# Kernel optimization log

Measured on AMD Instinct MI355X. Metric: run time of the kernel, lower is better.

Reference implementation:

```python
import jax, jax.numpy as jnp
import numpy as np
import math

N_EMBD = 1024
N_HEAD = 16
B, T = 2, 2048
MASK_VAL = -10.0  # non-standard soft mask value from original module


def setup_inputs() -> dict:
    key = jax.random.key(0)
    k1, k2, k3 = jax.random.split(key, 3)
    scale = 1.0 / math.sqrt(N_EMBD)
    x = jax.random.normal(k1, (B, T, N_EMBD), dtype=jnp.float32)
    # torch Linear weights: (out_features, in_features)
    w_attn = jax.random.normal(k2, (3 * N_EMBD, N_EMBD), dtype=jnp.float32) * scale
    w_proj = jax.random.normal(k3, (N_EMBD, N_EMBD), dtype=jnp.float32) * scale
    return {"x": x, "w_attn": w_attn, "w_proj": w_proj}


def reference(x, w_attn, w_proj):
    Bsz, Tlen, C = x.shape
    hs = C // N_HEAD
    qkv = jnp.einsum('btc,fc->btf', x, w_attn)  # [B,T,3C]
    q, k, v = jnp.split(qkv, 3, axis=-1)
    # [B,H,T,hs]
    q = q.reshape(Bsz, Tlen, N_HEAD, hs).transpose(0, 2, 1, 3)
    k = k.reshape(Bsz, Tlen, N_HEAD, hs).transpose(0, 2, 1, 3)
    v = v.reshape(Bsz, Tlen, N_HEAD, hs).transpose(0, 2, 1, 3)
    att = jnp.einsum('bhqd,bhkd->bhqk', q, k) * (1.0 / math.sqrt(hs))
    causal = jnp.tril(jnp.ones((Tlen, Tlen), dtype=bool))
    att = jnp.where(causal[None, None], att, MASK_VAL)
    att = jax.nn.softmax(att, axis=-1)
    y = jnp.einsum('bhqk,bhkd->bhqd', att, v)
    y = y.transpose(0, 2, 1, 3).reshape(Bsz, Tlen, C)
    return jnp.einsum('btc,fc->btf', y, w_proj)
```

## Files before the change

kernel.cpp:

```cpp
#include <hip/hip_runtime.h>
#include <hip/hip_bf16.h>
#include <stdint.h>

#define BSZ   2
#define TT    2048
#define NH    16
#define HS    64
#define CC    1024
#define C3    3072
#define MT    4096
#define E10   4.5399929762484854e-05f
#define SCL2  0.1803368801111204f

typedef __bf16 bf16;
typedef __bf16 bf16x8 __attribute__((ext_vector_type(8)));
typedef float  f32x4  __attribute__((ext_vector_type(4)));
typedef short  s16x4  __attribute__((ext_vector_type(4)));

#define AS1 __attribute__((address_space(1)))
#define AS3 __attribute__((address_space(3)))

__device__ __forceinline__ void glds16(const bf16* g, bf16* l) {
    __builtin_amdgcn_global_load_lds((const AS1 void*)g, (AS3 void*)l, 16, 0, 0);
}

#define NX8  (MT * CC / 8)
#define NWA8 (C3 * CC / 8)
#define NWP8 (CC * CC / 8)
__global__ __launch_bounds__(256)
void convert_all(const float* __restrict__ x, const float* __restrict__ wa,
                 const float* __restrict__ wp, bf16* __restrict__ xd,
                 bf16* __restrict__ wad, bf16* __restrict__ wpd,
                 int* __restrict__ flag) {
    __shared__ int wsum[4];
    const int tid = threadIdx.x;
    const uint16_t* x16 = (const uint16_t*)x;
    int local = 0;
    {
        uint16_t u = x16[tid];
        int e = (u >> 7) & 0xFF; local += (e >= 96 && e <= 159);
        u = x16[tid + 256];
        e = (u >> 7) & 0xFF; local += (e >= 96 && e <= 159);
    }
    local += __shfl_xor(local, 1, 64);
    local += __shfl_xor(local, 2, 64);
    local += __shfl_xor(local, 4, 64);
    local += __shfl_xor(local, 8, 64);
    local += __shfl_xor(local, 16, 64);
    local += __shfl_xor(local, 32, 64);
    if ((tid & 63) == 0) wsum[tid >> 6] = local;
    __syncthreads();
    const int cnt = wsum[0] + wsum[1] + wsum[2] + wsum[3];
    const int f = (cnt >= 461) ? 0 : 1;
    if (blockIdx.x == 0 && tid == 0) *flag = f;
    if (f == 0) return;

    long i = (long)blockIdx.x * 256 + tid;
    const float* s; bf16* d; long off;
    if (i < NX8)             { s = x;  d = xd;  off = i; }
    else if (i < NX8 + NWA8) { s = wa; d = wad; off = i - NX8; }
    else                     { s = wp; d = wpd; off = i - NX8 - NWA8; }
    const float4* sp = reinterpret_cast<const float4*>(s) + off * 2;
    float4 a = sp[0], b = sp[1];
    bf16x8 r;
    r[0] = (bf16)a.x; r[1] = (bf16)a.y; r[2] = (bf16)a.z; r[3] = (bf16)a.w;
    r[4] = (bf16)b.x; r[5] = (bf16)b.y; r[6] = (bf16)b.z; r[7] = (bf16)b.w;
    reinterpret_cast<bf16x8*>(d)[off] = r;
}

__global__ __launch_bounds__(256)
void gemm_bt(const bf16* __restrict__ A0, const bf16* __restrict__ A1,
             const bf16* __restrict__ B0, const bf16* __restrict__ B1,
             void* __restrict__ Cmain, bf16* __restrict__ Cv,
             float* __restrict__ Vtile,
             const int* __restrict__ flag,
             int M, int N, int K, int lda, int ldb, int ldc,
             int split_col, int cf32_dyn) {
    __shared__ bf16 As[2][128 * 32];
    __shared__ bf16 Bs[2][128 * 32];

    const int f = *flag;
    const bf16* A = f ? A1 : A0;
    const bf16* B = f ? B1 : B0;
    const int cf32 = cf32_dyn & f;

    const int tid  = threadIdx.x;
    const int lane = tid & 63;
    const int wave = tid >> 6;
    const int wm   = wave >> 1;
    const int wn   = wave & 1;
    const int quad = lane >> 4;
    const int l16  = lane & 15;

    const int row0 = blockIdx.y * 128;
    const int col0 = blockIdx.x * 128;

    const int srow = tid >> 2;
    const int skk  = (tid & 3) * 8;

    const bf16* Ap = A + (long)(row0 + srow) * lda + skk;
    const bf16* Bp = B + (long)(col0 + srow) * ldb + skk;

    auto stage = [&](int k0, int buf) {
        glds16(Ap + k0,                  &As[buf][wave * 512]);
        glds16(Ap + (long)64 * lda + k0, &As[buf][wave * 512 + 2048]);
        glds16(Bp + k0,                  &Bs[buf][wave * 512]);
        glds16(Bp + (long)64 * ldb + k0, &Bs[buf][wave * 512 + 2048]);
    };

    f32x4 acc[4][4] = {};
    stage(0, 0);

    for (int k0 = 0; k0 < K; k0 += 32) {
        const int buf = (k0 >> 5) & 1;
        __syncthreads();
        if (k0 + 32 < K) stage(k0 + 32, buf ^ 1);

        const bf16* Ac = As[buf];
        const bf16* Bc = Bs[buf];
        bf16x8 af[4], bfv[4];
#pragma unroll
        for (int mi = 0; mi < 4; ++mi)
            af[mi] = *reinterpret_cast<const bf16x8*>(&Ac[(wm * 64 + mi * 16 + l16) * 32 + quad * 8]);
#pragma unroll
        for (int ni = 0; ni < 4; ++ni)
            bfv[ni] = *reinterpret_cast<const bf16x8*>(&Bc[(wn * 64 + ni * 16 + l16) * 32 + quad * 8]);
#pragma unroll
        for (int mi = 0; mi < 4; ++mi)
#pragma unroll
            for (int ni = 0; ni < 4; ++ni)
                acc[mi][ni] = __builtin_amdgcn_mfma_f32_16x16x32_bf16(af[mi], bfv[ni], acc[mi][ni], 0, 0, 0);
    }

    if (split_col < 0 || col0 < split_col) {
#pragma unroll
        for (int mi = 0; mi < 4; ++mi)
#pragma unroll
            for (int ni = 0; ni < 4; ++ni)
#pragma unroll
                for (int r = 0; r < 4; ++r) {
                    int row = row0 + wm * 64 + mi * 16 + quad * 4 + r;
                    int col = col0 + wn * 64 + ni * 16 + l16;
                    float v = acc[mi][ni][r];
                    if (cf32) ((float*)Cmain)[(long)row * ldc + col] = v;
                    else      ((bf16*)Cmain)[(long)row * ldc + col] = (bf16)v;
                }
    } else {
        const int h  = (col0 - split_col + wn * 64) >> 6;
        const int bq = row0 >> 11;
        const int tc = ((row0 & 2047) >> 6) + wm;
#pragma unroll
        for (int ni = 0; ni < 4; ++ni) {
            long vrow = (long)(bq * NH + h) * 64 + ni * 16 + l16;
#pragma unroll
            for (int mi = 0; mi < 4; ++mi) {
                bf16 outv[4];
#pragma unroll
                for (int r = 0; r < 4; ++r) outv[r] = (bf16)acc[mi][ni][r];
                *reinterpret_cast<uint2*>(&Cv[vrow * 2048 + tc * 64 + quad * 16 + mi * 4]) =
                    *reinterpret_cast<uint2*>(outv);
            }
        }
#pragma unroll
        for (int ni = 0; ni < 4; ++ni) {
            float s = 0.f;
#pragma unroll
            for (int mi = 0; mi < 4; ++mi)
#pragma unroll
                for (int r = 0; r < 4; ++r) s += acc[mi][ni][r];
            s += __shfl_xor(s, 16, 64);
            s += __shfl_xor(s, 32, 64);
            if (quad == 0)
                Vtile[((long)(bq * NH + h) * 32 + tc) * 64 + ni * 16 + l16] = s;
        }
    }
}

__global__ __launch_bounds__(256)
void gemm_bt64(const bf16* __restrict__ A0, const bf16* __restrict__ A1,
               const bf16* __restrict__ B0, const bf16* __restrict__ B1,
               void* __restrict__ C, const int* __restrict__ flag,
               int M, int N, int K, int lda, int ldb, int ldc, int cf32_dyn) {
    __shared__ bf16 As[2][128 * 32];
    __shared__ bf16 Bs[2][64 * 32];

    const int f = *flag;
    const bf16* A = f ? A1 : A0;
    const bf16* B = f ? B1 : B0;
    const int cf32 = cf32_dyn & f;

    const int tid  = threadIdx.x;
    const int lane = tid & 63;
    const int wave = tid >> 6;
    const int wm   = wave >> 1;
    const int wn   = wave & 1;
    const int quad = lane >> 4;
    const int l16  = lane & 15;

    const int row0 = blockIdx.y * 128;
    const int col0 = blockIdx.x * 64;

    const int srow = tid >> 2;
    const int skk  = (tid & 3) * 8;

    const bf16* Ap = A + (long)(row0 + srow) * lda + skk;
    const bf16* Bp = B + (long)(col0 + srow) * ldb + skk;

    auto stage = [&](int k0, int buf) {
        glds16(Ap + k0,                  &As[buf][wave * 512]);
        glds16(Ap + (long)64 * lda + k0, &As[buf][wave * 512 + 2048]);
        glds16(Bp + k0,                  &Bs[buf][wave * 512]);
    };

    f32x4 acc[4][2] = {};
    stage(0, 0);

    for (int k0 = 0; k0 < K; k0 += 32) {
        const int buf = (k0 >> 5) & 1;
        __syncthreads();
        if (k0 + 32 < K) stage(k0 + 32, buf ^ 1);

        const bf16* Ac = As[buf];
        const bf16* Bc = Bs[buf];
        bf16x8 af[4], bfv[2];
#pragma unroll
        for (int mi = 0; mi < 4; ++mi)
            af[mi] = *reinterpret_cast<const bf16x8*>(&Ac[(wm * 64 + mi * 16 + l16) * 32 + quad * 8]);
#pragma unroll
        for (int ni = 0; ni < 2; ++ni)
            bfv[ni] = *reinterpret_cast<const bf16x8*>(&Bc[(wn * 32 + ni * 16 + l16) * 32 + quad * 8]);
#pragma unroll
        for (int mi = 0; mi < 4; ++mi)
#pragma unroll
            for (int ni = 0; ni < 2; ++ni)
                acc[mi][ni] = __builtin_amdgcn_mfma_f32_16x16x32_bf16(af[mi], bfv[ni], acc[mi][ni], 0, 0, 0);
    }

#pragma unroll
    for (int mi = 0; mi < 4; ++mi)
#pragma unroll
        for (int ni = 0; ni < 2; ++ni)
#pragma unroll
            for (int r = 0; r < 4; ++r) {
                int row = row0 + wm * 64 + mi * 16 + quad * 4 + r;
                int col = col0 + wn * 32 + ni * 16 + l16;
                float v = acc[mi][ni][r];
                if (cf32) ((float*)C)[(long)row * ldc + col] = v;
                else      ((bf16*)C)[(long)row * ldc + col] = (bf16)v;
            }
}

__global__ void vts_suffix(const float* __restrict__ Vtile, float* __restrict__ Vts) {
    const int bh = blockIdx.x, d = threadIdx.x;
    Vts[((long)bh * 33 + 32) * 64 + d] = 0.f;
    float acc = 0.f;
    for (int kt = 31; kt >= 0; --kt) {
        acc += Vtile[((long)bh * 32 + kt) * 64 + d];
        Vts[((long)bh * 33 + kt) * 64 + d] = acc;
    }
}

__global__ __launch_bounds__(256, 3)
void attn(bf16* __restrict__ qk, const bf16* __restrict__ Vt,
          const float* __restrict__ Vts) {
    __shared__ bf16 Ks[3][64 * 64];
    __shared__ bf16 Vs[3][64 * 64];

    const int tid  = threadIdx.x;
    const int lane = tid & 63;
    const int wave = tid >> 6;
    const int quad = lane >> 4;
    const int l16  = lane & 15;

    const int f2   = blockIdx.x;
    const int xcd  = f2 & 7;
    const int slot = f2 >> 3;
    const int u    = slot & 3;
    const int chunk = 31 - (slot >> 2);
    const int h = xcd * 2 + (u & 1);
    const int b = u >> 1;
    const int bh = b * 16 + h;
    const int q0 = chunk * 64;
    const long rbase = (long)b * TT;
    const int ktend = chunk + 1;

    const bf16* qp = qk + (rbase + q0 + wave * 16 + l16) * 2048 + h * HS;
    bf16x8 qf0 = *reinterpret_cast<const bf16x8*>(qp + quad * 8);
    bf16x8 qf1 = *reinterpret_cast<const bf16x8*>(qp + 32 + quad * 8);

    f32x4 O[4] = {};
    float lp = 0.f;

    const int rl  = lane >> 3;
    const int cs  = (lane & 7) ^ rl;
    const int row0dma = wave * 16 + rl;
    const bf16* kgb = qk + (rbase + row0dma) * 2048 + CC + h * HS + cs * 8;
    const bf16* vgb = Vt + ((long)(b * NH + h) * 64 + row0dma) * 2048 + cs * 8;
    const int sx = l16 & 7;

    auto stage = [&](int kt, int bi) {
        glds16(kgb + (long)(kt * 64) * 2048,     &Ks[bi][wave * 1024]);
        glds16(kgb + (long)(kt * 64 + 8) * 2048, &Ks[bi][wave * 1024 + 512]);
        glds16(vgb + kt * 64,                    &Vs[bi][wave * 1024]);
        glds16(vgb + 8 * 2048 + kt * 64,         &Vs[bi][wave * 1024 + 512]);
    };

    auto qkTile = [&](int bi, f32x4* Sn) {
        const bf16* Kc = Ks[bi];
        bf16x8 kf0[4], kf1[4];
#pragma unroll
        for (int g = 0; g < 4; ++g) {
            const int krow = g * 16 + l16;
            kf0[g] = *reinterpret_cast<const bf16x8*>(&Kc[krow * 64 + ((quad ^ sx) * 8)]);
            kf1[g] = *reinterpret_cast<const bf16x8*>(&Kc[krow * 64 + (((4 + quad) ^ sx) * 8)]);
        }
        __builtin_amdgcn_s_setprio(1);
#pragma unroll
        for (int g = 0; g < 4; ++g) {
            Sn[g] = __builtin_amdgcn_mfma_f32_16x16x32_bf16(kf0[g], qf0, Sn[g], 0, 0, 0);
            Sn[g] = __builtin_amdgcn_mfma_f32_16x16x32_bf16(kf1[g], qf1, Sn[g], 0, 0, 0);
        }
        __builtin_amdgcn_s_setprio(0);
    };
    auto vTile = [&](int bi, s16x4 vf[4][4]) {
        const bf16* Vc = Vs[bi];
#pragma unroll
        for (int dg = 0; dg < 4; ++dg) {
            const int vrow = dg * 16 + l16;
            union { uint4 u4; s16x4 s[2]; } ua, ub;
            ua.u4 = *reinterpret_cast<const uint4*>(&Vc[vrow * 64 + (((2 * quad) ^ sx) * 8)]);
            ub.u4 = *reinterpret_cast<const uint4*>(&Vc[vrow * 64 + (((2 * quad + 1) ^ sx) * 8)]);
            vf[dg][0] = ua.s[0]; vf[dg][1] = ua.s[1];
            vf[dg][2] = ub.s[0]; vf[dg][3] = ub.s[1];
        }
    };

    stage(0, 0);
    stage(ktend > 1 ? 1 : 0, 1);
    asm volatile("s_waitcnt vmcnt(4)" ::: "memory");
    __builtin_amdgcn_s_barrier();
    __builtin_amdgcn_sched_barrier(0);

    f32x4 Sc[4] = {};
    s16x4 vc[4][4] = {};
    qkTile(0, Sc);
    vTile(0, vc);

    int rb = 1;
    int sb = 2;
    for (int kt = 0; kt < ktend; ++kt) {
        int nkt = kt + 2; nkt = (nkt < ktend) ? nkt : (ktend - 1);
        stage(nkt, sb);
        asm volatile("s_waitcnt vmcnt(4)" ::: "memory");
        __builtin_amdgcn_s_barrier();
        __builtin_amdgcn_sched_barrier(0);

        f32x4 Sn[4] = {};
        s16x4 vn[4][4] = {};
        if (kt + 1 < ktend) {
            qkTile(rb, Sn);
            vTile(rb, vn);
        }

        const bool dtile = (kt == ktend - 1);
        const int ql = wave * 16 + l16;
        s16x4 pk[4];
#pragma unroll
        for (int g = 0; g < 4; ++g) {
#pragma unroll
            for (int r = 0; r < 4; ++r) {
                float p = __builtin_exp2f(Sc[g][r] * SCL2);
                if (dtile) {
                    int kl = g * 16 + quad * 4 + r;
                    p = (kl > ql) ? E10 : p;
                }
                lp += p;
                union { bf16 b_; short s_; } u2;
                u2.b_ = (bf16)p;
                pk[g][r] = u2.s_;
            }
        }

        __builtin_amdgcn_s_setprio(1);
#pragma unroll
        for (int dg = 0; dg < 4; ++dg) {
            O[dg] = __builtin_amdgcn_mfma_f32_16x16x16bf16_1k(vc[dg][0], pk[0], O[dg], 0, 0, 0);
            O[dg] = __builtin_amdgcn_mfma_f32_16x16x16bf16_1k(vc[dg][1], pk[1], O[dg], 0, 0, 0);
            O[dg] = __builtin_amdgcn_mfma_f32_16x16x16bf16_1k(vc[dg][2], pk[2], O[dg], 0, 0, 0);
            O[dg] = __builtin_amdgcn_mfma_f32_16x16x16bf16_1k(vc[dg][3], pk[3], O[dg], 0, 0, 0);
        }
        __builtin_amdgcn_s_setprio(0);

#pragma unroll
        for (int g = 0; g < 4; ++g) Sc[g] = Sn[g];
#pragma unroll
        for (int dg = 0; dg < 4; ++dg)
#pragma unroll
            for (int j = 0; j < 4; ++j) vc[dg][j] = vn[dg][j];

        rb = (rb == 2) ? 0 : rb + 1;
        sb = (sb == 2) ? 0 : sb + 1;
    }

    lp += __shfl_xor(lp, 16, 64);
    lp += __shfl_xor(lp, 32, 64);

    const int nfut = TT - ktend * 64;
    const float l = lp + (float)nfut * E10;
    const float invl = 1.0f / l;
    const float* vfp = Vts + ((long)bh * 33 + ktend) * 64;

    bf16* yp = qk + (rbase + q0 + wave * 16 + l16) * 2048 + h * HS;
#pragma unroll
    for (int dg = 0; dg < 4; ++dg) {
        bf16 outv[4];
#pragma unroll
        for (int r = 0; r < 4; ++r) {
            float o = O[dg][r] + E10 * vfp[dg * 16 + quad * 4 + r];
            outv[r] = (bf16)(o * invl);
        }
        *reinterpret_cast<uint2*>(yp + dg * 16 + quad * 4) =
            *reinterpret_cast<uint2*>(outv);
    }
}

extern "C" void kernel_launch(void* const* d_in, const int* in_sizes, int n_in,
                              void* d_out, int out_size, void* d_ws, size_t ws_size,
                              hipStream_t stream) {
    const void* x      = d_in[0];
    const void* w_attn = d_in[1];
    const void* w_proj = d_in[2];

    char* ws = (char*)d_ws;
    bf16*  qk     = (bf16*)ws;
    bf16*  Vt     = (bf16*)(ws + (size_t)MT * 2048 * 2);
    char*  p2     = ws + (size_t)MT * 2048 * 2 + (size_t)32 * 64 * 2048 * 2;
    int*   flag   = (int*)p2;
    float* Vts    = (float*)(p2 + 256);
    bf16*  wp_cvt = (bf16*)(p2 + 256 + 32 * 33 * 64 * 4);
    float* Vtile  = (float*)((char*)wp_cvt + (size_t)CC * CC * 2);

    bf16* x_cvt  = (bf16*)d_out;
    bf16* wa_cvt = (bf16*)d_out + (size_t)MT * CC;

    convert_all<<<(NX8 + NWA8 + NWP8) / 256, 256, 0, stream>>>(
        (const float*)x, (const float*)w_attn, (const float*)w_proj,
        x_cvt, wa_cvt, wp_cvt, flag);

    gemm_bt<<<dim3(C3 / 128, MT / 128), 256, 0, stream>>>(
        (const bf16*)x, x_cvt, (const bf16*)w_attn, wa_cvt, qk, Vt, Vtile, flag,
        MT, C3, CC, CC, CC, 2048, 2048, 0);

    vts_suffix<<<dim3(BSZ * NH), dim3(64), 0, stream>>>(Vtile, Vts);

    attn<<<dim3(1024), 256, 0, stream>>>(qk, Vt, Vts);

    gemm_bt64<<<dim3(CC / 64, MT / 128), 256, 0, stream>>>(
        qk, qk, (const bf16*)w_proj, wp_cvt, d_out, flag,
        MT, CC, CC, 2048, CC, CC, 1);
}
```

Measured before the change: 177.9 us.

## Fuse V-suffix sum into attention, compute row sums via MFMA, prescale Q

```diff
diff --git a/kernel.cpp b/kernel.cpp
--- a/kernel.cpp
+++ b/kernel.cpp
@@ -250,21 +250,12 @@
             }
 }
 
-__global__ void vts_suffix(const float* __restrict__ Vtile, float* __restrict__ Vts) {
-    const int bh = blockIdx.x, d = threadIdx.x;
-    Vts[((long)bh * 33 + 32) * 64 + d] = 0.f;
-    float acc = 0.f;
-    for (int kt = 31; kt >= 0; --kt) {
-        acc += Vtile[((long)bh * 32 + kt) * 64 + d];
-        Vts[((long)bh * 33 + kt) * 64 + d] = acc;
-    }
-}
-
 __global__ __launch_bounds__(256, 3)
 void attn(bf16* __restrict__ qk, const bf16* __restrict__ Vt,
-          const float* __restrict__ Vts) {
+          const float* __restrict__ Vtile) {
     __shared__ bf16 Ks[3][64 * 64];
     __shared__ bf16 Vs[3][64 * 64];
+    __shared__ float Vpart[4][64];
 
     const int tid  = threadIdx.x;
     const int lane = tid & 63;
@@ -287,9 +278,16 @@
     const bf16* qp = qk + (rbase + q0 + wave * 16 + l16) * 2048 + h * HS;
     bf16x8 qf0 = *reinterpret_cast<const bf16x8*>(qp + quad * 8);
     bf16x8 qf1 = *reinterpret_cast<const bf16x8*>(qp + 32 + quad * 8);
+#pragma unroll
+    for (int j = 0; j < 8; ++j) {
+        qf0[j] = (bf16)((float)qf0[j] * SCL2);
+        qf1[j] = (bf16)((float)qf1[j] * SCL2);
+    }
 
     f32x4 O[4] = {};
-    float lp = 0.f;
+    f32x4 lpacc = {};
+    const short one_bf16 = (short)0x3F80;
+    const s16x4 ones = {one_bf16, one_bf16, one_bf16, one_bf16};
 
     const int rl  = lane >> 3;
     const int cs  = (lane & 7) ^ rl;
@@ -369,12 +367,11 @@
         for (int g = 0; g < 4; ++g) {
 #pragma unroll
             for (int r = 0; r < 4; ++r) {
-                float p = __builtin_exp2f(Sc[g][r] * SCL2);
+                float p = __builtin_exp2f(Sc[g][r]);
                 if (dtile) {
                     int kl = g * 16 + quad * 4 + r;
                     p = (kl > ql) ? E10 : p;
                 }
-                lp += p;
                 union { bf16 b_; short s_; } u2;
                 u2.b_ = (bf16)p;
                 pk[g][r] = u2.s_;
@@ -389,6 +386,10 @@
             O[dg] = __builtin_amdgcn_mfma_f32_16x16x16bf16_1k(vc[dg][2], pk[2], O[dg], 0, 0, 0);
             O[dg] = __builtin_amdgcn_mfma_f32_16x16x16bf16_1k(vc[dg][3], pk[3], O[dg], 0, 0, 0);
         }
+        lpacc = __builtin_amdgcn_mfma_f32_16x16x16bf16_1k(ones, pk[0], lpacc, 0, 0, 0);
+        lpacc = __builtin_amdgcn_mfma_f32_16x16x16bf16_1k(ones, pk[1], lpacc, 0, 0, 0);
+        lpacc = __builtin_amdgcn_mfma_f32_16x16x16bf16_1k(ones, pk[2], lpacc, 0, 0, 0);
+        lpacc = __builtin_amdgcn_mfma_f32_16x16x16bf16_1k(ones, pk[3], lpacc, 0, 0, 0);
         __builtin_amdgcn_s_setprio(0);
 
 #pragma unroll
@@ -402,13 +403,17 @@
         sb = (sb == 2) ? 0 : sb + 1;
     }
 
-    lp += __shfl_xor(lp, 16, 64);
-    lp += __shfl_xor(lp, 32, 64);
+    {
+        float s = 0.f;
+        for (int kt = ktend + wave; kt < 32; kt += 4)
+            s += Vtile[((long)bh * 32 + kt) * 64 + lane];
+        Vpart[wave][lane] = s;
+    }
+    __syncthreads();
 
     const int nfut = TT - ktend * 64;
-    const float l = lp + (float)nfut * E10;
+    const float l = lpacc[0] + (float)nfut * E10;
     const float invl = 1.0f / l;
-    const float* vfp = Vts + ((long)bh * 33 + ktend) * 64;
 
     bf16* yp = qk + (rbase + q0 + wave * 16 + l16) * 2048 + h * HS;
 #pragma unroll
@@ -416,7 +421,9 @@
         bf16 outv[4];
 #pragma unroll
         for (int r = 0; r < 4; ++r) {
-            float o = O[dg][r] + E10 * vfp[dg * 16 + quad * 4 + r];
+            const int d = dg * 16 + quad * 4 + r;
+            float vts = Vpart[0][d] + Vpart[1][d] + Vpart[2][d] + Vpart[3][d];
+            float o = O[dg][r] + E10 * vts;
             outv[r] = (bf16)(o * invl);
         }
         *reinterpret_cast<uint2*>(yp + dg * 16 + quad * 4) =
@@ -436,7 +443,6 @@
     bf16*  Vt     = (bf16*)(ws + (size_t)MT * 2048 * 2);
     char*  p2     = ws + (size_t)MT * 2048 * 2 + (size_t)32 * 64 * 2048 * 2;
     int*   flag   = (int*)p2;
-    float* Vts    = (float*)(p2 + 256);
     bf16*  wp_cvt = (bf16*)(p2 + 256 + 32 * 33 * 64 * 4);
     float* Vtile  = (float*)((char*)wp_cvt + (size_t)CC * CC * 2);
 
@@ -451,9 +457,7 @@
         (const bf16*)x, x_cvt, (const bf16*)w_attn, wa_cvt, qk, Vt, Vtile, flag,
         MT, C3, CC, CC, CC, 2048, 2048, 0);
 
-    vts_suffix<<<dim3(BSZ * NH), dim3(64), 0, stream>>>(Vtile, Vts);
-
-    attn<<<dim3(1024), 256, 0, stream>>>(qk, Vt, Vts);
+    attn<<<dim3(1024), 256, 0, stream>>>(qk, Vt, Vtile);
 
     gemm_bt64<<<dim3(CC / 64, MT / 128), 256, 0, stream>>>(
         qk, qk, (const bf16*)w_proj, wp_cvt, d_out, flag,
```

Measured after the change: 177.2 us. About the same (-0.4%).
